# Optimization experiments

Hardware: AMD Instinct MI355X
Metric: run time of the kernel (lower is better)

## Reference

```python
import jax, jax.numpy as jnp
import numpy as np

N = 100000   # total atoms
M = 12       # neighbors per atom
C = 2000     # crystals
ORIG = 92    # original atom feature len
NBR = 41     # edge (Gaussian distance) feature len
F = 64       # atom_fea_len
H = 128      # h_fea_len
NCONV = 3
EPS = 1e-5


def setup_inputs() -> dict:
    key = jax.random.key(0)
    ks = jax.random.split(key, 12)
    def w(k, shape, fan_in):
        return (jax.random.normal(k, shape, jnp.float32) / np.sqrt(fan_in)).astype(jnp.float32)
    inp = {}
    inp["atom_fea"] = jax.random.normal(ks[0], (N, ORIG), jnp.float32)
    inp["nbr_fea"] = jax.random.normal(ks[1], (N, M, NBR), jnp.float32)
    inp["nbr_fea_idx"] = jax.random.randint(ks[2], (N, M), 0, N)
    inp["crystal_ids"] = jnp.sort(jax.random.randint(ks[3], (N,), 0, C))
    inp["emb_W"] = w(ks[4], (ORIG, F), ORIG)
    inp["emb_b"] = jnp.zeros((F,), jnp.float32)
    inp["conv_W"] = w(ks[5], (NCONV, 2 * F + NBR, 2 * F), 2 * F + NBR)
    inp["conv_b"] = jnp.zeros((NCONV, 2 * F), jnp.float32)
    inp["bn1_g"] = jnp.ones((NCONV, 2 * F), jnp.float32)
    inp["bn1_b"] = jnp.zeros((NCONV, 2 * F), jnp.float32)
    inp["bn2_g"] = jnp.ones((NCONV, F), jnp.float32)
    inp["bn2_b"] = jnp.zeros((NCONV, F), jnp.float32)
    inp["W3_W"] = w(ks[6], (F, F), F)
    inp["W3_b"] = jnp.zeros((F,), jnp.float32)
    inp["fc_W"] = w(ks[7], (F, H), F)
    inp["fc_b"] = jnp.zeros((H,), jnp.float32)
    inp["out_W"] = w(ks[8], (H, 1), H)
    inp["out_b"] = jnp.zeros((1,), jnp.float32)
    return inp


def _bn(x, g, b):
    # BatchNorm1d in training mode: batch mean, biased variance
    m = jnp.mean(x, axis=0)
    v = jnp.var(x, axis=0)
    return (x - m) * jax.lax.rsqrt(v + EPS) * g + b


def _seg_mean(x, ids, num):
    s = jax.ops.segment_sum(x, ids, num_segments=num)          # [num, F]
    cnt = jax.ops.segment_sum(jnp.ones((x.shape[0], 1), x.dtype), ids, num_segments=num)
    return s / jnp.maximum(cnt, 1.0)


def _conv_layer(x, nbr_fea, nbr_idx, W, b, g1, b1, g2, b2):
    n, m = nbr_idx.shape
    atom_nbr = x[nbr_idx]                                      # [N, M, F] gather
    self_fea = jnp.broadcast_to(x[:, None, :], (n, m, x.shape[1]))
    total = jnp.concatenate([self_fea, atom_nbr, nbr_fea], axis=2)  # [N, M, 2F+NBR]
    gated = total @ W + b                                      # [N, M, 2F]
    gated = _bn(gated.reshape(-1, 2 * F), g1, b1).reshape(n, m, 2 * F)
    nbr_filter = jax.nn.sigmoid(gated[..., :F])
    nbr_core = jnp.tanh(gated[..., F:])
    nbr_sumed = jnp.sum(nbr_filter * nbr_core, axis=1)          # [N, F]
    nbr_sumed = _bn(nbr_sumed, g2, b2)
    return jnp.tanh(x + nbr_sumed)


def reference(atom_fea, nbr_fea, nbr_fea_idx, crystal_ids,
              emb_W, emb_b, conv_W, conv_b, bn1_g, bn1_b, bn2_g, bn2_b,
              W3_W, W3_b, fc_W, fc_b, out_W, out_b):
    x = atom_fea @ emb_W + emb_b                               # [N, F]
    for i in range(NCONV):
        x = _conv_layer(x, nbr_fea, nbr_fea_idx, conv_W[i], conv_b[i],
                        bn1_g[i], bn1_b[i], bn2_g[i], bn2_b[i])
    # pooling(): per-crystal mean expanded back to each atom
    crys_mean = _seg_mean(x, crystal_ids, C)                   # [C, F]
    v_ = crys_mean[crystal_ids]                                # [N, F]
    c = jnp.tanh(v_ @ W3_W + W3_b)                             # [N, F]
    a = jax.nn.sigmoid(jnp.sum(x * c, axis=1, keepdims=True))  # [N, 1]
    crys_fea = _seg_mean(a * x, crystal_ids, C)                # [C, F]
    crys_fea = jax.nn.softplus(crys_fea @ fc_W + fc_b)         # [C, H]
    out = crys_fea @ out_W + out_b                             # [C, 1]
    return out, x
```

## Files before the change

### kernel.cpp

```cpp
#include <hip/hip_runtime.h>
#include <hip/hip_bf16.h>


#define NA    100000
#define MN    12
#define NC    2000
#define ORIGF 92
#define NBRF  41
#define FD    64
#define NBLK  3125
#define EPSF  1e-5f

#define REP28(X) X(0)X(1)X(2)X(3)X(4)X(5)X(6)X(7)X(8)X(9)X(10)X(11)X(12)X(13)X(14)X(15)X(16)X(17)X(18)X(19)X(20)X(21)X(22)X(23)X(24)X(25)X(26)X(27)
#define REP41(X) X(0)X(1)X(2)X(3)X(4)X(5)X(6)X(7)X(8)X(9)X(10)X(11)X(12)X(13)X(14)X(15)X(16)X(17)X(18)X(19)X(20)X(21)X(22)X(23)X(24)X(25)X(26)X(27)X(28)X(29)X(30)X(31)X(32)X(33)X(34)X(35)X(36)X(37)X(38)X(39)X(40)
#define REP64(X) X(0)X(1)X(2)X(3)X(4)X(5)X(6)X(7)X(8)X(9)X(10)X(11)X(12)X(13)X(14)X(15)X(16)X(17)X(18)X(19)X(20)X(21)X(22)X(23)X(24)X(25)X(26)X(27)X(28)X(29)X(30)X(31)X(32)X(33)X(34)X(35)X(36)X(37)X(38)X(39)X(40)X(41)X(42)X(43)X(44)X(45)X(46)X(47)X(48)X(49)X(50)X(51)X(52)X(53)X(54)X(55)X(56)X(57)X(58)X(59)X(60)X(61)X(62)X(63)

typedef const float* fp;

__device__ __forceinline__ float rlf(float v, int q){
  return __int_as_float(__builtin_amdgcn_readlane(__float_as_int(v), q));
}
__device__ __forceinline__ float fsig(float z){
  z = fminf(fmaxf(z, -30.f), 30.f);
  return 1.f / (1.f + __expf(-z));
}
__device__ __forceinline__ float ftanh(float z){
  z = fminf(fmaxf(z, -15.f), 15.f);
  float e = __expf(2.f * z);
  return (e - 1.f) / (e + 1.f);
}

__global__ void zero_kernel(float* __restrict__ p, int n){
  for (int i = blockIdx.x * blockDim.x + threadIdx.x; i < n; i += gridDim.x * blockDim.x)
    p[i] = 0.f;
}

__global__ __launch_bounds__(256, 2) void emb_kernel(
    fp __restrict__ af, fp __restrict__ W, fp __restrict__ b,
    float* __restrict__ x)
{
  const int lane = threadIdx.x & 63, w = threadIdx.x >> 6;
#define EA(k) float wa##k = W[k * FD + lane];
  REP64(EA)
#undef EA
#define EB(k) float wb##k = W[(k + 64) * FD + lane];
  REP28(EB)
#undef EB
  const float bias = b[lane];
  const int base = blockIdx.x * 32 + w * 8;
  #pragma unroll 1
  for (int it = 0; it < 8; ++it){
    const int i = base + it;
    float ev0 = af[i * ORIGF + lane];
    float ev1 = (lane < 28) ? af[i * ORIGF + 64 + lane] : 0.f;
    float acc = bias;
#define FA(k) acc = fmaf(rlf(ev0, k), wa##k, acc);
    REP64(FA)
#undef FA
#define FB(k) acc = fmaf(rlf(ev1, k), wb##k, acc);
    REP28(FB)
#undef FB
    x[i * FD + lane] = acc;
  }
}

__global__ __launch_bounds__(256, 4) void stw_kernel(
    const float* __restrict__ xin, fp __restrict__ W, fp __restrict__ bias,
    float* __restrict__ out)
{
  const int lane = threadIdx.x & 63, w = threadIdx.x >> 6;
  const int ch = (w & 1) * 64 + lane;
#define SW(k) float wv##k = W[k * 128 + ch];
  REP64(SW)
#undef SW
  const float bb = bias ? bias[ch] : 0.f;
  const int base = blockIdx.x * 32 + (w >> 1) * 16;
  #pragma unroll 1
  for (int it = 0; it < 16; ++it){
    const int i = base + it;
    float xv = xin[i * FD + lane];
    float acc = bb;
#define SF(k) acc = fmaf(rlf(xv, k), wv##k, acc);
    REP64(SF)
#undef SF
    out[i * 128 + ch] = acc;
  }
}

__global__ __launch_bounds__(256, 2) void edge_stats_kernel(
    const float* __restrict__ S, const float* __restrict__ T,
    fp __restrict__ nbr, const int* __restrict__ idx,
    fp __restrict__ We, float* __restrict__ p1)
{
  const int lane = threadIdx.x & 63, w = threadIdx.x >> 6;
  const int clo = lane, chi = lane + 64;
#define DW(q) float wlo##q = We[q * 128 + clo], whi##q = We[q * 128 + chi];
  REP41(DW)
#undef DW
  float sum_lo = 0.f, ssq_lo = 0.f, sum_hi = 0.f, ssq_hi = 0.f;
  const int base = blockIdx.x * 32 + w * 8;
  #pragma unroll 1
  for (int it = 0; it < 8; ++it){
    const int i = base + it;
    const float slo = S[i * 128 + clo];
    const float shi = S[i * 128 + chi];
    int kk = (lane < MN) ? idx[i * MN + lane] : 0;
    fp nb = nbr + (size_t)i * (MN * NBRF);
    int k0 = __builtin_amdgcn_readlane(kk, 0);
    float tlo = T[k0 * 128 + clo];
    float thi = T[k0 * 128 + chi];
    float ev  = (lane < NBRF) ? nb[lane] : 0.f;
    #pragma unroll 1
    for (int j = 0; j < MN; j++){
      float tlo_n = 0.f, thi_n = 0.f, ev_n = 0.f;
      if (j + 1 < MN){
        int kn = __builtin_amdgcn_readlane(kk, j + 1);
        tlo_n = T[kn * 128 + clo];
        thi_n = T[kn * 128 + chi];
        ev_n  = (lane < NBRF) ? nb[(j + 1) * NBRF + lane] : 0.f;
      }
      float glo = slo + tlo, ghi = shi + thi;
#define EF(q) { float s_ = rlf(ev, q); glo = fmaf(s_, wlo##q, glo); ghi = fmaf(s_, whi##q, ghi); }
      REP41(EF)
#undef EF
      sum_lo += glo; ssq_lo = fmaf(glo, glo, ssq_lo);
      sum_hi += ghi; ssq_hi = fmaf(ghi, ghi, ssq_hi);
      tlo = tlo_n; thi = thi_n; ev = ev_n;
    }
  }
  __shared__ float red[4 * 512];
  red[w * 512 + 2 * clo    ] = sum_lo;
  red[w * 512 + 2 * clo + 1] = ssq_lo;
  red[w * 512 + 2 * chi    ] = sum_hi;
  red[w * 512 + 2 * chi + 1] = ssq_hi;
  __syncthreads();
  const int t = threadIdx.x;
  const int ch = t & 127, which = t >> 7;
  float v = 0.f;
  #pragma unroll
  for (int ww = 0; ww < 4; ++ww) v += red[ww * 512 + 2 * ch + which];
  p1[blockIdx.x * 256 + t] = v;
}

__global__ __launch_bounds__(256, 4) void edge_stats_store_kernel(
    const float* __restrict__ S, const float* __restrict__ T,
    fp __restrict__ nbr, const int* __restrict__ idx,
    fp __restrict__ We, float* __restrict__ p1, float* __restrict__ gated)
{
  const int lane = threadIdx.x & 63, w = threadIdx.x >> 6;
  const int half = w & 1;
  const int ch = half * 64 + lane;
#define DW(q) float wv##q = We[q * 128 + ch];
  REP41(DW)
#undef DW
#define PIN(q) asm volatile("" : "+v"(wv##q));
  REP41(PIN)
#undef PIN
  float sum = 0.f, ssq = 0.f;
  const int base = blockIdx.x * 32 + (w >> 1) * 16;
  #pragma unroll 1
  for (int it = 0; it < 16; ++it){
    const int i = base + it;
    const float sv = S[i * 128 + ch];
    int kk = (lane < MN) ? idx[i * MN + lane] : 0;
    fp nb = nbr + (size_t)i * (MN * NBRF);
    float* gb = gated + (((size_t)i * MN) << 7) + ch;
    int k0 = __builtin_amdgcn_readlane(kk, 0);
    float tv = T[k0 * 128 + ch];
    float ev = (lane < NBRF) ? nb[lane] : 0.f;
    #pragma unroll 1
    for (int j = 0; j < MN; j++){
      float tv_n = 0.f, ev_n = 0.f;
      if (j + 1 < MN){
        int kn = __builtin_amdgcn_readlane(kk, j + 1);
        tv_n = T[kn * 128 + ch];
        ev_n = (lane < NBRF) ? nb[(j + 1) * NBRF + lane] : 0.f;
      }
      float g = sv + tv;
#define EF(q) g = fmaf(rlf(ev, q), wv##q, g);
      REP41(EF)
#undef EF
      gb[(size_t)j << 7] = g;
      sum += g; ssq = fmaf(g, g, ssq);
      tv = tv_n; ev = ev_n;
    }
  }
  __shared__ float red[4 * 128];
  red[w * 128 + 2 * lane    ] = sum;
  red[w * 128 + 2 * lane + 1] = ssq;
  __syncthreads();
  const int t = threadIdx.x;
  const int c = t & 127, which = t >> 7;
  const int h = c >> 6, cl = c & 63;
  float v = red[h * 128 + 2 * cl + which] + red[(h + 2) * 128 + 2 * cl + which];
  p1[blockIdx.x * 256 + t] = v;
}

__global__ __launch_bounds__(256, 4) void edge_apply_load_kernel(
    const float* __restrict__ gated, const float* __restrict__ ss1,
    float* __restrict__ ns, float* __restrict__ p2)
{
  const int lane = threadIdx.x & 63, w = threadIdx.x >> 6;
  const float sc_lo = ss1[lane],      sh_lo = ss1[128 + lane];
  const float sc_hi = ss1[64 + lane], sh_hi = ss1[192 + lane];
  float sum2 = 0.f, ssq2 = 0.f;
  const int base = blockIdx.x * 32 + w * 8;
  #pragma unroll 1
  for (int it = 0; it < 8; ++it){
    const int i = base + it;
    fp gb = gated + (((size_t)i * MN) << 7);
    float acc = 0.f;
    #pragma unroll
    for (int j = 0; j < MN; ++j){
      float glo = gb[(j << 7) + lane];
      float ghi = gb[(j << 7) + 64 + lane];
      float filt = fsig(fmaf(glo, sc_lo, sh_lo));
      float core = ftanh(fmaf(ghi, sc_hi, sh_hi));
      acc = fmaf(filt, core, acc);
    }
    ns[i * FD + lane] = acc;
    sum2 += acc; ssq2 = fmaf(acc, acc, ssq2);
  }
  __shared__ float red[4 * 128];
  red[w * 128 + 2 * lane    ] = sum2;
  red[w * 128 + 2 * lane + 1] = ssq2;
  __syncthreads();
  const int t = threadIdx.x;
  if (t < 128){
    const int ch = t & 63, which = t >> 6;
    float v = 0.f;
    #pragma unroll
    for (int ww = 0; ww < 4; ++ww) v += red[ww * 128 + 2 * ch + which];
    p2[blockIdx.x * 128 + t] = v;
  }
}

__global__ __launch_bounds__(256, 2) void edge_apply_kernel(
    const float* __restrict__ S, const float* __restrict__ T,
    fp __restrict__ nbr, const int* __restrict__ idx,
    fp __restrict__ We, const float* __restrict__ ss1,
    float* __restrict__ ns, float* __restrict__ p2)
{
  const int lane = threadIdx.x & 63, w = threadIdx.x >> 6;
  const int clo = lane, chi = lane + 64;
#define DW(q) float wlo##q = We[q * 128 + clo], whi##q = We[q * 128 + chi];
  REP41(DW)
#undef DW
  const float sc_lo = ss1[clo],       sh_lo = ss1[128 + clo];
  const float sc_hi = ss1[chi],       sh_hi = ss1[128 + chi];
  float sum2 = 0.f, ssq2 = 0.f;
  const int base = blockIdx.x * 32 + w * 8;
  #pragma unroll 1
  for (int it = 0; it < 8; ++it){
    const int i = base + it;
    const float slo = S[i * 128 + clo];
    const float shi = S[i * 128 + chi];
    int kk = (lane < MN) ? idx[i * MN + lane] : 0;
    fp nb = nbr + (size_t)i * (MN * NBRF);
    int k0 = __builtin_amdgcn_readlane(kk, 0);
    float tlo = T[k0 * 128 + clo];
    float thi = T[k0 * 128 + chi];
    float ev  = (lane < NBRF) ? nb[lane] : 0.f;
    float acc = 0.f;
    #pragma unroll 1
    for (int j = 0; j < MN; j++){
      float tlo_n = 0.f, thi_n = 0.f, ev_n = 0.f;
      if (j + 1 < MN){
        int kn = __builtin_amdgcn_readlane(kk, j + 1);
        tlo_n = T[kn * 128 + clo];
        thi_n = T[kn * 128 + chi];
        ev_n  = (lane < NBRF) ? nb[(j + 1) * NBRF + lane] : 0.f;
      }
      float glo = slo + tlo, ghi = shi + thi;
#define EF(q) { float s_ = rlf(ev, q); glo = fmaf(s_, wlo##q, glo); ghi = fmaf(s_, whi##q, ghi); }
      REP41(EF)
#undef EF
      float filt = fsig(fmaf(glo, sc_lo, sh_lo));
      float core = ftanh(fmaf(ghi, sc_hi, sh_hi));
      acc = fmaf(filt, core, acc);
      tlo = tlo_n; thi = thi_n; ev = ev_n;
    }
    ns[i * FD + lane] = acc;
    sum2 += acc; ssq2 = fmaf(acc, acc, ssq2);
  }
  __shared__ float red[4 * 128];
  red[w * 128 + 2 * lane    ] = sum2;
  red[w * 128 + 2 * lane + 1] = ssq2;
  __syncthreads();
  const int t = threadIdx.x;
  if (t < 128){
    const int ch = t & 63, which = t >> 6;
    float v = 0.f;
    #pragma unroll
    for (int ww = 0; ww < 4; ++ww) v += red[ww * 128 + 2 * ch + which];
    p2[blockIdx.x * 128 + t] = v;
  }
}

__global__ void reduce_rows_kernel(const float* __restrict__ p, float* __restrict__ accum,
                                   int nrows, int ncols)
{
  const int t = threadIdx.x;
  float a = 0.f;
  for (int r = blockIdx.x; r < nrows; r += gridDim.x) a += p[r * ncols + t];
  atomicAdd(&accum[t], a);
}

__global__ void finalize1_kernel(const float* __restrict__ acc, fp g, fp b,
                                 float* __restrict__ ss1)
{
  const int c = threadIdx.x;
  const float inv = 1.f / 1200000.f;
  float mean = acc[c] * inv;
  float var  = fmaxf(acc[128 + c] * inv - mean * mean, 0.f);
  float sc   = g[c] * rsqrtf(var + EPSF);
  ss1[c] = sc;
  ss1[128 + c] = b[c] - mean * sc;
}

__global__ void finalize2_kernel(const float* __restrict__ acc, fp g, fp b,
                                 float* __restrict__ ss2)
{
  const int c = threadIdx.x;
  const float inv = 1.f / 100000.f;
  float mean = acc[c] * inv;
  float var  = fmaxf(acc[64 + c] * inv - mean * mean, 0.f);
  float sc   = g[c] * rsqrtf(var + EPSF);
  ss2[c] = sc;
  ss2[64 + c] = b[c] - mean * sc;
}

__global__ __launch_bounds__(256) void bn2res_kernel(
    float* __restrict__ x, const float* __restrict__ ns,
    const float* __restrict__ ss2, float* __restrict__ xout)
{
  const int e = (blockIdx.x * 256 + threadIdx.x) * 4;
  const int c = e & 63;
  float4 xv = *(const float4*)(x + e);
  float4 nv = *(const float4*)(ns + e);
  float r0 = ftanh(fmaf(nv.x, ss2[c + 0], ss2[64 + c + 0]) + xv.x);
  float r1 = ftanh(fmaf(nv.y, ss2[c + 1], ss2[64 + c + 1]) + xv.y);
  float r2 = ftanh(fmaf(nv.z, ss2[c + 2], ss2[64 + c + 2]) + xv.z);
  float r3 = ftanh(fmaf(nv.w, ss2[c + 3], ss2[64 + c + 3]) + xv.w);
  *(float4*)(x + e) = make_float4(r0, r1, r2, r3);
  if (xout){
    *(float4*)(xout + e) = make_float4(r0, r1, r2, r3);
  }
}

__global__ __launch_bounds__(256) void pool1_kernel(
    const float* __restrict__ x, const int* __restrict__ cid,
    float* __restrict__ csum, float* __restrict__ ccnt)
{
  const int lane = threadIdx.x & 63, w = threadIdx.x >> 6;
  const int wg = blockIdx.x * 4 + w;
  const int i0 = wg * 64;
  if (i0 >= NA) return;
  const int i1 = min(i0 + 64, NA);
  int cur = -1; float acc = 0.f; int run = 0;
  for (int i = i0; i < i1; ++i){
    int cd = cid[i];
    if (cd != cur){
      if (cur >= 0){
        atomicAdd(&csum[cur * FD + lane], acc);
        if (lane == 0) atomicAdd(&ccnt[cur], (float)run);
      }
      cur = cd; acc = 0.f; run = 0;
    }
    acc += x[i * FD + lane];
    run++;
  }
  if (cur >= 0){
    atomicAdd(&csum[cur * FD + lane], acc);
    if (lane == 0) atomicAdd(&ccnt[cur], (float)run);
  }
}

__global__ void cm3_kernel(const float* __restrict__ csum, const float* __restrict__ ccnt,
                           fp W3, fp b3, float* __restrict__ c3)
{
  const int b = blockIdx.x, t = threadIdx.x;
  __shared__ float mean[64];
  float inv = 1.f / fmaxf(ccnt[b], 1.f);
  mean[t] = csum[b * FD + t] * inv;
  __syncthreads();
  float acc = b3[t];
  #pragma unroll
  for (int k = 0; k < 64; k++) acc = fmaf(mean[k], W3[k * FD + t], acc);
  c3[b * FD + t] = ftanh(acc);
}

__global__ __launch_bounds__(256) void pool2_kernel(
    const float* __restrict__ x, const int* __restrict__ cid,
    const float* __restrict__ c3, float* __restrict__ cfs)
{
  const int lane = threadIdx.x & 63, w = threadIdx.x >> 6;
  const int wg = blockIdx.x * 4 + w;
  const int i0 = wg * 64;
  if (i0 >= NA) return;
  const int i1 = min(i0 + 64, NA);
  int cur = -1; float acc = 0.f;
  for (int i = i0; i < i1; ++i){
    int cd = cid[i];
    if (cd != cur){
      if (cur >= 0) atomicAdd(&cfs[cur * FD + lane], acc);
      cur = cd; acc = 0.f;
    }
    float xv = x[i * FD + lane];
    float p = xv * c3[cd * FD + lane];
    #pragma unroll
    for (int off = 32; off; off >>= 1) p += __shfl_xor(p, off);
    acc = fmaf(fsig(p), xv, acc);
  }
  if (cur >= 0) atomicAdd(&cfs[cur * FD + lane], acc);
}

__global__ void head_kernel(const float* __restrict__ cfs, const float* __restrict__ ccnt,
                            fp fcW, fp fcb, fp oW, fp ob,
                            float* __restrict__ outp)
{
  const int b = blockIdx.x, t = threadIdx.x;
  __shared__ float row[64];
  __shared__ float red[128];
  float inv = 1.f / fmaxf(ccnt[b], 1.f);
  if (t < 64) row[t] = cfs[b * FD + t] * inv;
  __syncthreads();
  float acc = fcb[t];
  #pragma unroll
  for (int k = 0; k < 64; k++) acc = fmaf(row[k], fcW[k * 128 + t], acc);
  float sp = (acc > 20.f) ? acc : log1pf(__expf(acc));
  red[t] = sp * oW[t];
  __syncthreads();
  for (int off = 64; off; off >>= 1){
    if (t < off) red[t] += red[t + off];
    __syncthreads();
  }
  if (t == 0) outp[b] = red[0] + ob[0];
}

static const size_t O_X    = 0;
static const size_t O_S    = 6400000;
static const size_t O_T    = 19200000;
static const size_t O_NS   = 32000000;
static const size_t O_P1   = 38400000;
static const size_t O_P2   = 39200000;
static const size_t O_SS1  = 39600000;
static const size_t O_SS2  = 39600256;
static const size_t O_G1   = 39600384;
static const size_t O_G2   = 39600640;
static const size_t O_CSUM = 39600768;
static const size_t O_CCNT = 39728768;
static const size_t O_C3   = 39730768;
static const size_t O_CFS  = 39858768;
static const size_t O_END  = 39986768;
static const size_t O_GATED= 39986768;
static const size_t O_END2 = 193586768;

extern "C" void kernel_launch(void* const* d_in, const int* in_sizes, int n_in,
                              void* d_out, int out_size, void* d_ws, size_t ws_size,
                              hipStream_t stream)
{
  (void)in_sizes; (void)n_in; (void)out_size;
  if (ws_size < O_END * sizeof(float)) return;
  const bool big = ws_size >= O_END2 * sizeof(float);

  fp atom_fea = (fp)d_in[0];
  fp nbr_fea  = (fp)d_in[1];
  const int* nbr_idx = (const int*)d_in[2];
  const int* cids    = (const int*)d_in[3];
  fp embW = (fp)d_in[4];
  fp embb = (fp)d_in[5];
  fp convW = (fp)d_in[6];
  fp convb = (fp)d_in[7];
  fp bn1g = (fp)d_in[8];
  fp bn1b = (fp)d_in[9];
  fp bn2g = (fp)d_in[10];
  fp bn2b = (fp)d_in[11];
  fp W3W  = (fp)d_in[12];
  fp W3b  = (fp)d_in[13];
  fp fcW  = (fp)d_in[14];
  fp fcb  = (fp)d_in[15];
  fp oW   = (fp)d_in[16];
  fp ob   = (fp)d_in[17];

  float* out_head = (float*)d_out;
  float* out_x    = out_head + NC;

  float* W  = (float*)d_ws;
  float* x    = W + O_X;
  float* S    = W + O_S;
  float* T    = W + O_T;
  float* ns   = W + O_NS;
  float* p1   = W + O_P1;
  float* p2   = W + O_P2;
  float* ss1  = W + O_SS1;
  float* ss2  = W + O_SS2;
  float* g1s  = W + O_G1;
  float* g2s  = W + O_G2;
  float* csum = W + O_CSUM;
  float* ccnt = W + O_CCNT;
  float* c3   = W + O_C3;
  float* cfs  = W + O_CFS;
  float* gated= W + O_GATED;

  zero_kernel<<<128, 256, 0, stream>>>(csum, 386000);

  emb_kernel<<<NBLK, 256, 0, stream>>>(atom_fea, embW, embb, x);

  for (int l = 0; l < 3; ++l){
    fp Wl = convW + (size_t)l * 169 * 128;
    stw_kernel<<<NBLK, 256, 0, stream>>>(x, Wl,            convb + l * 128, S);
    stw_kernel<<<NBLK, 256, 0, stream>>>(x, Wl + 64 * 128, (fp)nullptr,     T);
    zero_kernel<<<1, 256, 0, stream>>>(g1s, 384);
    if (big){
      edge_stats_store_kernel<<<NBLK, 256, 0, stream>>>(S, T, nbr_fea, nbr_idx, Wl + 128 * 128, p1, gated);
      reduce_rows_kernel<<<64, 256, 0, stream>>>(p1, g1s, NBLK, 256);
      finalize1_kernel<<<1, 128, 0, stream>>>(g1s, bn1g + l * 128, bn1b + l * 128, ss1);
      edge_apply_load_kernel<<<NBLK, 256, 0, stream>>>(gated, ss1, ns, p2);
    } else {
      edge_stats_kernel<<<NBLK, 256, 0, stream>>>(S, T, nbr_fea, nbr_idx, Wl + 128 * 128, p1);
      reduce_rows_kernel<<<64, 256, 0, stream>>>(p1, g1s, NBLK, 256);
      finalize1_kernel<<<1, 128, 0, stream>>>(g1s, bn1g + l * 128, bn1b + l * 128, ss1);
      edge_apply_kernel<<<NBLK, 256, 0, stream>>>(S, T, nbr_fea, nbr_idx, Wl + 128 * 128, ss1, ns, p2);
    }
    reduce_rows_kernel<<<64, 128, 0, stream>>>(p2, g2s, NBLK, 128);
    finalize2_kernel<<<1, 64, 0, stream>>>(g2s, bn2g + l * 64, bn2b + l * 64, ss2);
    bn2res_kernel<<<6250, 256, 0, stream>>>(x, ns, ss2, (l == 2) ? out_x : (float*)nullptr);
  }

  pool1_kernel<<<391, 256, 0, stream>>>(x, cids, csum, ccnt);
  cm3_kernel<<<NC, 64, 0, stream>>>(csum, ccnt, W3W, W3b, c3);
  pool2_kernel<<<391, 256, 0, stream>>>(x, cids, c3, cfs);
  head_kernel<<<NC, 128, 0, stream>>>(cfs, ccnt, fcW, fcb, oW, ob, out_head);
}
```

Measured before the change: 2.869 ms.

## Stage edge features in LDS and process four neighbors per iteration

The edge stats kernel now copies each atom's 12x41 edge feature block into per-wave shared memory. The inner loop then reads those values with broadcast LDS loads instead of 41 readlane ops per neighbor. The loop also handles four neighbors at once, which gives four independent FMA chains and four T gathers in flight. This trades the old software prefetch and readlane-heavy path for more LDS traffic and more live registers. The wave-local sync depends only on an lgkmcnt wait with no barrier, which relies on each wave using its own slice.

New measurement: 2.375 ms. 1.21x faster.

```diff
diff --git a/kernel.cpp b/kernel.cpp
--- a/kernel.cpp
+++ b/kernel.cpp
@@ -148,14 +148,11 @@
     fp __restrict__ We, float* __restrict__ p1, float* __restrict__ gated)
 {
   const int lane = threadIdx.x & 63, w = threadIdx.x >> 6;
-  const int half = w & 1;
-  const int ch = half * 64 + lane;
+  const int ch = (w & 1) * 64 + lane;
 #define DW(q) float wv##q = We[q * 128 + ch];
   REP41(DW)
 #undef DW
-#define PIN(q) asm volatile("" : "+v"(wv##q));
-  REP41(PIN)
-#undef PIN
+  __shared__ float elds[4][MN * NBRF];
   float sum = 0.f, ssq = 0.f;
   const int base = blockIdx.x * 32 + (w >> 1) * 16;
   #pragma unroll 1
@@ -164,25 +161,37 @@
     const float sv = S[i * 128 + ch];
     int kk = (lane < MN) ? idx[i * MN + lane] : 0;
     fp nb = nbr + (size_t)i * (MN * NBRF);
-    float* gb = gated + (((size_t)i * MN) << 7) + ch;
-    int k0 = __builtin_amdgcn_readlane(kk, 0);
-    float tv = T[k0 * 128 + ch];
-    float ev = (lane < NBRF) ? nb[lane] : 0.f;
+    #pragma unroll
+    for (int r = 0; r < 7; ++r) elds[w][r * 64 + lane] = nb[r * 64 + lane];
+    if (lane < MN * NBRF - 448) elds[w][448 + lane] = nb[448 + lane];
+    asm volatile("s_waitcnt lgkmcnt(0)" ::: "memory");
     #pragma unroll 1
-    for (int j = 0; j < MN; j++){
-      float tv_n = 0.f, ev_n = 0.f;
-      if (j + 1 < MN){
-        int kn = __builtin_amdgcn_readlane(kk, j + 1);
-        tv_n = T[kn * 128 + ch];
-        ev_n = (lane < NBRF) ? nb[(j + 1) * NBRF + lane] : 0.f;
-      }
-      float g = sv + tv;
-#define EF(q) g = fmaf(rlf(ev, q), wv##q, g);
+    for (int jg = 0; jg < MN / 4; ++jg){
+      const int j0 = jg * 4;
+      int k0 = __builtin_amdgcn_readlane(kk, j0);
+      int k1 = __builtin_amdgcn_readlane(kk, j0 + 1);
+      int k2 = __builtin_amdgcn_readlane(kk, j0 + 2);
+      int k3 = __builtin_amdgcn_readlane(kk, j0 + 3);
+      float g0 = sv + T[k0 * 128 + ch];
+      float g1 = sv + T[k1 * 128 + ch];
+      float g2 = sv + T[k2 * 128 + ch];
+      float g3 = sv + T[k3 * 128 + ch];
+      const float* eb = &elds[w][j0 * NBRF];
+#define EF(q) { float e0_ = eb[q]; float e1_ = eb[NBRF + q]; \
+                float e2_ = eb[2 * NBRF + q]; float e3_ = eb[3 * NBRF + q]; \
+                g0 = fmaf(e0_, wv##q, g0); g1 = fmaf(e1_, wv##q, g1); \
+                g2 = fmaf(e2_, wv##q, g2); g3 = fmaf(e3_, wv##q, g3); }
       REP41(EF)
 #undef EF
-      gb[(size_t)j << 7] = g;
-      sum += g; ssq = fmaf(g, g, ssq);
-      tv = tv_n; ev = ev_n;
+      float* gb = gated + (((size_t)(i * MN + j0)) << 7) + ch;
+      gb[0]   = g0;
+      gb[128] = g1;
+      gb[256] = g2;
+      gb[384] = g3;
+      sum += g0; ssq = fmaf(g0, g0, ssq);
+      sum += g1; ssq = fmaf(g1, g1, ssq);
+      sum += g2; ssq = fmaf(g2, g2, ssq);
+      sum += g3; ssq = fmaf(g3, g3, ssq);
     }
   }
   __shared__ float red[4 * 128];
```
